# Performance work log

Measured on AMD Instinct MI355X. Metric: run time of the kernel, lower is better.

Reference implementation:

```python
import jax, jax.numpy as jnp
import numpy as np

N_NODES = 32768
NUM_EDGES = 524288
NUM_GRAPHS = 32
C = 128            # hidden channels
N_LAYERS = 3       # len(hidden_channels)-1
D_IN = 144         # 4 (op embedding dim) + 140
C_MID = 80         # mem1 out
C_OUT = 64         # mem2 out / classes
H1, K1N = 5, 10    # mem1 heads / clusters
H2, K2N = 5, 1     # mem2 heads / clusters
EPS = 1e-15


def _gatv2(x, src, dst, Wl, bl, Wr, br, att, cb):
    """GATv2Conv (heads=1, negative_slope=0.2), edges src->dst incl. self loops."""
    n = x.shape[0]
    xl = x @ Wl + bl                                  # source transform [N,C]
    xr = x @ Wr + br                                  # target transform [N,C]
    e = (jax.nn.leaky_relu(xl[src] + xr[dst], 0.2) @ att)  # [E]
    m = jax.ops.segment_max(e, dst, num_segments=n)   # segment softmax over in-edges
    ee = jnp.exp(e - m[dst])
    denom = jax.ops.segment_sum(ee, dst, num_segments=n)
    alpha = ee / denom[dst]
    out = jax.ops.segment_sum(alpha[:, None] * xl[src], dst, num_segments=n)
    return out + cb


def _bn(h, gamma, beta):
    # BatchNorm1d with batch statistics (training-mode forward), eps=1e-5
    mu = h.mean(0)
    var = h.var(0)
    return (h - mu) * jax.lax.rsqrt(var + 1e-5) * gamma + beta


def _mem_pool(xd, Kmem, W):
    # xd [B,N,C], Kmem [H,K,C]; Student-t kernel, tau=1 -> (1+d)^-1
    d = (jnp.sum(xd * xd, -1)[:, :, None, None]
         + jnp.sum(Kmem * Kmem, -1)[None, None]
         - 2.0 * jnp.einsum('bnc,hkc->bnhk', xd, Kmem))  # [B,N,H,K] sq. distances
    S = 1.0 / (1.0 + d)
    S = S / S.sum(-1, keepdims=True)   # normalize over clusters
    S = S.mean(2)                      # average heads -> [B,N,K]
    out = jnp.einsum('bnk,bnc->bkc', S, xd) @ W
    return out, S


def _kl_loss(S):
    S2 = S * S / S.sum(1, keepdims=True)
    den = S2.sum(2, keepdims=True)
    den = jnp.where(S.sum(2, keepdims=True) == 0.0, 1.0, den)
    P = jnp.maximum(S2 / den, EPS)
    Sc = jnp.maximum(S, EPS)
    # KLDivLoss(reduction='batchmean'), input = log(S)
    return jnp.sum(P * (jnp.log(P) - jnp.log(Sc))) / S.shape[0]


def setup_inputs():
    key = jax.random.key(0)
    ks = jax.random.split(key, 24)
    x = jax.random.normal(ks[0], (N_NODES, D_IN), jnp.float32)
    edge_index = jax.random.randint(ks[1], (2, NUM_EDGES), 0, N_NODES, jnp.int32)
    batch = (jnp.arange(N_NODES, dtype=jnp.int32) // (N_NODES // NUM_GRAPHS))
    s = 1.0 / np.sqrt(C)
    inp = {
        'x': x, 'edge_index': edge_index, 'batch': batch,
        'W_in': jax.random.normal(ks[2], (D_IN, C), jnp.float32) / np.sqrt(D_IN),
        'b_in': jnp.zeros((C,), jnp.float32),
        'bn_gamma': jnp.ones((N_LAYERS, C), jnp.float32),
        'bn_beta': jnp.zeros((N_LAYERS, C), jnp.float32),
        'Wl': jax.random.normal(ks[3], (N_LAYERS, C, C), jnp.float32) * s,
        'bl': jnp.zeros((N_LAYERS, C), jnp.float32),
        'Wr': jax.random.normal(ks[4], (N_LAYERS, C, C), jnp.float32) * s,
        'br': jnp.zeros((N_LAYERS, C), jnp.float32),
        'att': jax.random.normal(ks[5], (N_LAYERS, C), jnp.float32) * s,
        'conv_bias': jnp.zeros((N_LAYERS, C), jnp.float32),
        'K1': jax.random.normal(ks[6], (H1, K1N, C), jnp.float32),
        'Wm1': jax.random.normal(ks[7], (C, C_MID), jnp.float32) * s,
        'K2': jax.random.normal(ks[8], (H2, K2N, C_MID), jnp.float32),
        'Wm2': jax.random.normal(ks[9], (C_MID, C_OUT), jnp.float32) / np.sqrt(C_MID),
    }
    return inp


def reference(x, edge_index, batch, W_in, b_in, bn_gamma, bn_beta,
              Wl, bl, Wr, br, att, conv_bias, K1, Wm1, K2, Wm2):
    h = x @ W_in + b_in                               # self.linear
    loops = jnp.arange(N_NODES, dtype=edge_index.dtype)
    src = jnp.concatenate([edge_index[0], loops])     # GATv2 add_self_loops=True
    dst = jnp.concatenate([edge_index[1], loops])
    for l in range(N_LAYERS):                         # DeepGCNLayer block='res+'
        t = _bn(h, bn_gamma[l], bn_beta[l])
        t = jax.nn.leaky_relu(t, 0.01)
        # dropout: identity (deterministic reference)
        t = _gatv2(t, src, dst, Wl[l], bl[l], Wr[l], br[l], att[l], conv_bias[l])
        h = h + t
    per = N_NODES // NUM_GRAPHS
    xd = h.reshape(NUM_GRAPHS, per, C)                # to_dense_batch (equal-size graphs)
    x1, S1 = _mem_pool(xd, K1, Wm1)                   # [B,10,80]
    x1 = jax.nn.leaky_relu(x1, 0.01)
    x2, S2 = _mem_pool(x1, K2, Wm2)                   # [B,1,64]
    logits = jax.nn.log_softmax(x2.squeeze(1), -1)    # [B,64]
    return logits, _kl_loss(S1) + _kl_loss(S2)
```

## Files before the change

kernel.cpp:

```cpp
#include <hip/hip_runtime.h>
#include <math.h>

#define N_NODES   32768
#define NUM_EDGES 524288
#define NUM_GRAPHS 32
#define PER_G     1024
#define C         128
#define D_IN      144
#define C_MID     80
#define C_OUT     64
#define NL        3

#define WS_H    0
#define WS_XL   16777216
#define WS_XR   25165824
#define WS_CSR  33554432
#define WS_DEG  35651584
#define WS_OFF  35782656
#define WS_CUR  35913728
#define WS_BNP  36044800
#define WS_SC   38141952
#define WS_SH   38142464
#define WS_S1   38142976
#define WS_CS   39453696
#define WS_PP   39454976
#define WS_X1   44697856
#define WS_KL   44800256

using short8 = __attribute__((ext_vector_type(8))) short;
using f32x4  = __attribute__((ext_vector_type(4))) float;

__device__ __forceinline__ float wave_sum(float v) {
  #pragma unroll
  for (int m = 1; m < 64; m <<= 1) v += __shfl_xor(v, m, 64);
  return v;
}

__device__ __forceinline__ float lrelu2(float v) { return fmaxf(v, 0.2f * v); }

__device__ __forceinline__ unsigned short f2bf(float f) {
  union { float f; unsigned u; } c; c.f = f;
  unsigned r = (c.u + 0x7FFFu + ((c.u >> 16) & 1u)) >> 16;
  return (unsigned short)r;
}
__device__ __forceinline__ float bflo(unsigned u) {
  union { unsigned u; float f; } c; c.u = u << 16; return c.f;
}
__device__ __forceinline__ float bfhi(unsigned u) {
  union { unsigned u; float f; } c; c.u = u & 0xFFFF0000u; return c.f;
}

__global__ void k_count(const int* __restrict__ dst, int* __restrict__ deg) {
  int e = blockIdx.x * 256 + threadIdx.x;
  if (e < NUM_EDGES) atomicAdd(&deg[dst[e]], 1);
}

__global__ __launch_bounds__(1024) void k_scan(const int* __restrict__ deg, int* __restrict__ off) {
  __shared__ int part[1024];
  int t = threadIdx.x;
  int base = t * 32;
  int s = 0;
  #pragma unroll
  for (int i = 0; i < 32; i++) s += deg[base + i];
  part[t] = s;
  __syncthreads();
  for (int d = 1; d < 1024; d <<= 1) {
    int v = (t >= d) ? part[t - d] : 0;
    __syncthreads();
    part[t] += v;
    __syncthreads();
  }
  int run = (t == 0) ? 0 : part[t - 1];
  for (int i = 0; i < 32; i++) { off[base + i] = run; run += deg[base + i]; }
}

__global__ void k_fill(const int* __restrict__ src, const int* __restrict__ dst,
                       const int* __restrict__ off, int* __restrict__ cur,
                       int* __restrict__ csr) {
  int e = blockIdx.x * 256 + threadIdx.x;
  if (e < NUM_EDGES) {
    int d = dst[e];
    int p = atomicAdd(&cur[d], 1);
    csr[off[d] + p] = src[e];
  }
}

__global__ __launch_bounds__(256) void k_lin_mfma(const float* __restrict__ x,
    const float* __restrict__ W, const float* __restrict__ bias, float* __restrict__ h) {
  __shared__ __align__(16) char smem[61440];
  char* tA = smem;
  char* tB = smem + 20480;
  int n0 = blockIdx.x * 64;
  int tid = threadIdx.x;
  for (int t = 0; t < 32; t++) {
    int cp = tid & 127;
    int node = t * 2 + (tid >> 7);
    if (cp < 80) {
      unsigned pkv = 0;
      if (cp < 72) {
        float2 xv = *(const float2*)&x[(size_t)(n0 + node) * D_IN + 2 * cp];
        pkv = ((unsigned)f2bf(xv.y) << 16) | f2bf(xv.x);
      }
      int byte = node * 320 + ((4 * cp) ^ ((node & 3) << 4));
      *(unsigned*)(tA + byte) = pkv;
    }
  }
  {
    int col = tid & 127, hh = tid >> 7;
    for (int t = 0; t < 40; t++) {
      int kp = t * 2 + hh;
      float w0 = (2 * kp < D_IN) ? W[(size_t)(2 * kp) * C + col] : 0.f;
      float w1 = (2 * kp + 1 < D_IN) ? W[(size_t)(2 * kp + 1) * C + col] : 0.f;
      unsigned pkv = ((unsigned)f2bf(w1) << 16) | f2bf(w0);
      int byte = col * 320 + ((4 * kp) ^ ((col & 3) << 4));
      *(unsigned*)(tB + byte) = pkv;
    }
  }
  __syncthreads();
  int l = tid & 63, w = tid >> 6;
  f32x4 acc[8];
  #pragma unroll
  for (int f = 0; f < 8; f++) acc[f] = (f32x4){0.f, 0.f, 0.f, 0.f};
  int arow = w * 16 + (l & 15);
  #pragma unroll
  for (int ks = 0; ks < 5; ks++) {
    int kb = ks * 64 + (l >> 4) * 16;
    short8 a = *(const short8*)(tA + arow * 320 + (kb ^ ((arow & 3) << 4)));
    #pragma unroll
    for (int f = 0; f < 8; f++) {
      int col = f * 16 + (l & 15);
      short8 b = *(const short8*)(tB + col * 320 + (kb ^ ((col & 3) << 4)));
      acc[f] = __builtin_amdgcn_mfma_f32_16x16x32_bf16(a, b, acc[f], 0, 0, 0);
    }
  }
  int rowb = n0 + w * 16 + (l >> 4) * 4;
  #pragma unroll
  for (int f = 0; f < 8; f++) {
    int col = f * 16 + (l & 15);
    float bv = bias[col];
    #pragma unroll
    for (int r = 0; r < 4; r++)
      h[(size_t)(rowb + r) * C + col] = acc[f][r] + bv;
  }
}

__global__ __launch_bounds__(128) void k_bn_part(const float* __restrict__ h, float* __restrict__ part) {
  int b = blockIdx.x; int c = threadIdx.x;
  float s = 0.f, s2 = 0.f;
  int r0 = b * 128;
  for (int r = 0; r < 128; r++) {
    float v = h[(size_t)(r0 + r) * C + c];
    s += v; s2 += v * v;
  }
  part[b * C + c] = s;
  part[256 * C + b * C + c] = s2;
}

__global__ __launch_bounds__(1024) void k_bn_fin(const float* __restrict__ part,
    const float* __restrict__ gamma, const float* __restrict__ beta,
    float* __restrict__ sc, float* __restrict__ sh) {
  __shared__ float ls[8 * 128];
  __shared__ float ls2[8 * 128];
  int c = threadIdx.x & 127, g = threadIdx.x >> 7;
  float s = 0.f, s2 = 0.f;
  for (int i = 0; i < 32; i++) {
    int b = g * 32 + i;
    s += part[b * C + c];
    s2 += part[256 * C + b * C + c];
  }
  ls[g * 128 + c] = s;
  ls2[g * 128 + c] = s2;
  __syncthreads();
  if (g == 0) {
    double S = 0.0, S2 = 0.0;
    #pragma unroll
    for (int k = 0; k < 8; k++) { S += ls[k * 128 + c]; S2 += ls2[k * 128 + c]; }
    double m = S / (double)N_NODES;
    double var = S2 / (double)N_NODES - m * m;
    float rsig = (float)(1.0 / sqrt(var + 1e-5));
    float scv = rsig * gamma[c];
    sc[c] = scv;
    sh[c] = beta[c] - (float)m * scv;
  }
}

__device__ __forceinline__ void gemm_half(const char* tA, const char* tB,
    const float* bias, unsigned short* out, int n0, int tid) {
  int l = tid & 63, w = tid >> 6;
  f32x4 acc[8];
  #pragma unroll
  for (int f = 0; f < 8; f++) acc[f] = (f32x4){0.f, 0.f, 0.f, 0.f};
  int arow = w * 16 + (l & 15);
  #pragma unroll
  for (int ks = 0; ks < 4; ks++) {
    int kb = ks * 64 + (l >> 4) * 16;
    short8 a = *(const short8*)(tA + arow * 256 + (kb ^ ((arow & 7) << 4)));
    #pragma unroll
    for (int f = 0; f < 8; f++) {
      int col = f * 16 + (l & 15);
      short8 b = *(const short8*)(tB + col * 256 + (kb ^ ((col & 7) << 4)));
      acc[f] = __builtin_amdgcn_mfma_f32_16x16x32_bf16(a, b, acc[f], 0, 0, 0);
    }
  }
  int rowb = n0 + w * 16 + (l >> 4) * 4;
  #pragma unroll
  for (int f = 0; f < 8; f++) {
    int col = f * 16 + (l & 15);
    float bv = bias[col];
    #pragma unroll
    for (int r = 0; r < 4; r++)
      out[(size_t)(rowb + r) * C + col] = f2bf(acc[f][r] + bv);
  }
}

__device__ __forceinline__ void stage_B(char* tB, const float* __restrict__ W, int tid) {
  int col = tid & 127, hh = tid >> 7;
  for (int t = 0; t < 32; t++) {
    int kp = t * 2 + hh;
    float w0 = W[(size_t)(2 * kp) * C + col];
    float w1 = W[(size_t)(2 * kp + 1) * C + col];
    unsigned pkv = ((unsigned)f2bf(w1) << 16) | f2bf(w0);
    int byte = col * 256 + ((4 * kp) ^ ((col & 7) << 4));
    *(unsigned*)(tB + byte) = pkv;
  }
}

__global__ __launch_bounds__(256) void k_gemm_mfma(const float* __restrict__ h,
    const float* __restrict__ sc, const float* __restrict__ sh,
    const float* __restrict__ Wl, const float* __restrict__ bl,
    const float* __restrict__ Wr, const float* __restrict__ br,
    unsigned short* __restrict__ xl, unsigned short* __restrict__ xr) {
  __shared__ __align__(16) char smem[49152];
  char* tA = smem;
  char* tB = smem + 16384;
  int n0 = blockIdx.x * 64;
  int tid = threadIdx.x;
  for (int t = 0; t < 16; t++) {
    int item = t * 256 + tid;
    int node = item >> 6;
    int cp = item & 63;
    float2 hv = *(const float2*)&h[(size_t)(n0 + node) * C + 2 * cp];
    float2 scv = *(const float2*)&sc[2 * cp];
    float2 shv = *(const float2*)&sh[2 * cp];
    float t0 = hv.x * scv.x + shv.x; t0 = fmaxf(t0, 0.01f * t0);
    float t1 = hv.y * scv.y + shv.y; t1 = fmaxf(t1, 0.01f * t1);
    unsigned pkv = ((unsigned)f2bf(t1) << 16) | f2bf(t0);
    int byte = node * 256 + ((4 * cp) ^ ((node & 7) << 4));
    *(unsigned*)(tA + byte) = pkv;
  }
  stage_B(tB, Wl, tid);
  __syncthreads();
  gemm_half(tA, tB, bl, xl, n0, tid);
  __syncthreads();
  stage_B(tB, Wr, tid);
  __syncthreads();
  gemm_half(tA, tB, br, xr, n0, tid);
}

__global__ __launch_bounds__(256) void k_gat(float* __restrict__ h,
    const unsigned* __restrict__ xlb, const unsigned* __restrict__ xrb,
    const float* __restrict__ att, const float* __restrict__ cb,
    const int* __restrict__ off, const int* __restrict__ deg,
    const int* __restrict__ csr) {
  int tid = threadIdx.x;
  int lane = tid & 63;
  int w = tid >> 6;
  int half = lane >> 5;
  int q = lane & 31;
  int node = blockIdx.x * 8 + w * 2 + half;
  float4 a = *(const float4*)&att[q * 4];
  uint2 ur = *(const uint2*)&xrb[(size_t)node * 64 + q * 2];
  float xr0 = bflo(ur.x), xr1 = bfhi(ur.x), xr2 = bflo(ur.y), xr3 = bfhi(ur.y);
  uint2 us = *(const uint2*)&xlb[(size_t)node * 64 + q * 2];
  float acc0 = bflo(us.x), acc1 = bfhi(us.x), acc2 = bflo(us.y), acc3 = bfhi(us.y);
  float p0 = lrelu2(acc0 + xr0) * a.x + lrelu2(acc1 + xr1) * a.y
           + lrelu2(acc2 + xr2) * a.z + lrelu2(acc3 + xr3) * a.w;
  #pragma unroll
  for (int mm = 1; mm < 32; mm <<= 1) p0 += __shfl_xor(p0, mm, 64);
  float m = p0;
  float ssum = 1.f;
  int o = off[node], dg = deg[node];
  int dgmax = max(dg, __shfl_xor(dg, 32, 64));
  for (int j = 0; j < dgmax; j += 4) {
    int i0 = o + ((j + 0 < dg) ? j + 0 : 0);
    int i1 = o + ((j + 1 < dg) ? j + 1 : 0);
    int i2 = o + ((j + 2 < dg) ? j + 2 : 0);
    int i3 = o + ((j + 3 < dg) ? j + 3 : 0);
    int s0 = csr[i0], s1 = csr[i1], s2 = csr[i2], s3 = csr[i3];
    uint2 u0 = *(const uint2*)&xlb[(size_t)s0 * 64 + q * 2];
    uint2 u1 = *(const uint2*)&xlb[(size_t)s1 * 64 + q * 2];
    uint2 u2 = *(const uint2*)&xlb[(size_t)s2 * 64 + q * 2];
    uint2 u3 = *(const uint2*)&xlb[(size_t)s3 * 64 + q * 2];
    float y00 = bflo(u0.x), y01 = bfhi(u0.x), y02 = bflo(u0.y), y03 = bfhi(u0.y);
    float y10 = bflo(u1.x), y11 = bfhi(u1.x), y12 = bflo(u1.y), y13 = bfhi(u1.y);
    float y20 = bflo(u2.x), y21 = bfhi(u2.x), y22 = bflo(u2.y), y23 = bfhi(u2.y);
    float y30 = bflo(u3.x), y31 = bfhi(u3.x), y32 = bflo(u3.y), y33 = bfhi(u3.y);
    float t0 = lrelu2(y00 + xr0) * a.x + lrelu2(y01 + xr1) * a.y
             + lrelu2(y02 + xr2) * a.z + lrelu2(y03 + xr3) * a.w;
    float t1 = lrelu2(y10 + xr0) * a.x + lrelu2(y11 + xr1) * a.y
             + lrelu2(y12 + xr2) * a.z + lrelu2(y13 + xr3) * a.w;
    float t2 = lrelu2(y20 + xr0) * a.x + lrelu2(y21 + xr1) * a.y
             + lrelu2(y22 + xr2) * a.z + lrelu2(y23 + xr3) * a.w;
    float t3 = lrelu2(y30 + xr0) * a.x + lrelu2(y31 + xr1) * a.y
             + lrelu2(y32 + xr2) * a.z + lrelu2(y33 + xr3) * a.w;
    #pragma unroll
    for (int mm = 1; mm < 32; mm <<= 1) {
      t0 += __shfl_xor(t0, mm, 64);
      t1 += __shfl_xor(t1, mm, 64);
      t2 += __shfl_xor(t2, mm, 64);
      t3 += __shfl_xor(t3, mm, 64);
    }
    t0 = (j + 0 < dg) ? t0 : -1e30f;
    t1 = (j + 1 < dg) ? t1 : -1e30f;
    t2 = (j + 2 < dg) ? t2 : -1e30f;
    t3 = (j + 3 < dg) ? t3 : -1e30f;
    {
      float nm = fmaxf(m, t0); float f = __expf(m - nm); float p = __expf(t0 - nm);
      ssum = fmaf(ssum, f, p);
      acc0 = fmaf(acc0, f, p * y00); acc1 = fmaf(acc1, f, p * y01);
      acc2 = fmaf(acc2, f, p * y02); acc3 = fmaf(acc3, f, p * y03);
      m = nm;
    }
    {
      float nm = fmaxf(m, t1); float f = __expf(m - nm); float p = __expf(t1 - nm);
      ssum = fmaf(ssum, f, p);
      acc0 = fmaf(acc0, f, p * y10); acc1 = fmaf(acc1, f, p * y11);
      acc2 = fmaf(acc2, f, p * y12); acc3 = fmaf(acc3, f, p * y13);
      m = nm;
    }
    {
      float nm = fmaxf(m, t2); float f = __expf(m - nm); float p = __expf(t2 - nm);
      ssum = fmaf(ssum, f, p);
      acc0 = fmaf(acc0, f, p * y20); acc1 = fmaf(acc1, f, p * y21);
      acc2 = fmaf(acc2, f, p * y22); acc3 = fmaf(acc3, f, p * y23);
      m = nm;
    }
    {
      float nm = fmaxf(m, t3); float f = __expf(m - nm); float p = __expf(t3 - nm);
      ssum = fmaf(ssum, f, p);
      acc0 = fmaf(acc0, f, p * y30); acc1 = fmaf(acc1, f, p * y31);
      acc2 = fmaf(acc2, f, p * y32); acc3 = fmaf(acc3, f, p * y33);
      m = nm;
    }
  }
  float inv = 1.f / ssum;
  float4 cbv = *(const float4*)&cb[q * 4];
  float4 hv = *(float4*)&h[(size_t)node * C + q * 4];
  hv.x += acc0 * inv + cbv.x;
  hv.y += acc1 * inv + cbv.y;
  hv.z += acc2 * inv + cbv.z;
  hv.w += acc3 * inv + cbv.w;
  *(float4*)&h[(size_t)node * C + q * 4] = hv;
}

__global__ __launch_bounds__(320) void k_mem1(const float* __restrict__ h,
    const float* __restrict__ K1, float* __restrict__ S1, float* __restrict__ colsum) {
  __shared__ float dd[64 * 51];
  __shared__ float kn[50];
  int tid = threadIdx.x;
  int lane = tid & 63;
  int w = tid >> 6;
  int n0 = blockIdx.x * 64;
  if (tid < 50) {
    const float4* kr = reinterpret_cast<const float4*>(K1 + tid * C);
    float s = 0.f;
    for (int q = 0; q < 32; q++) {
      float4 kv = kr[q];
      s += kv.x * kv.x + kv.y * kv.y + kv.z * kv.z + kv.w * kv.w;
    }
    kn[tid] = s;
  }
  int wu = __builtin_amdgcn_readfirstlane(w);
  const float4* x4 = reinterpret_cast<const float4*>(h + (size_t)(n0 + lane) * C);
  const float4* K4 = reinterpret_cast<const float4*>(K1);
  float acc[10];
  #pragma unroll
  for (int it = 0; it < 10; it++) acc[it] = 0.f;
  float xn = 0.f;
  for (int q = 0; q < 32; q += 2) {
    float4 xa = x4[q], xb = x4[q + 1];
    xn += xa.x * xa.x + xa.y * xa.y + xa.z * xa.z + xa.w * xa.w
        + xb.x * xb.x + xb.y * xb.y + xb.z * xb.z + xb.w * xb.w;
    #pragma unroll
    for (int it = 0; it < 10; it++) {
      int j = wu + 5 * it;
      float4 ka = K4[j * 32 + q], kb = K4[j * 32 + q + 1];
      acc[it] += xa.x * ka.x + xa.y * ka.y + xa.z * ka.z + xa.w * ka.w
               + xb.x * kb.x + xb.y * kb.y + xb.z * kb.z + xb.w * kb.w;
    }
  }
  #pragma unroll
  for (int it = 0; it < 10; it++) dd[lane * 51 + wu + 5 * it] = acc[it];
  __syncthreads();
  if (tid < 64) {
    float sn[10];
    #pragma unroll
    for (int k = 0; k < 10; k++) sn[k] = 0.f;
    #pragma unroll
    for (int hd = 0; hd < 5; hd++) {
      float sh_[10]; float hs = 0.f;
      #pragma unroll
      for (int k = 0; k < 10; k++) {
        int j = hd * 10 + k;
        float dist = xn + kn[j] - 2.f * dd[tid * 51 + j];
        float s = 1.f / (1.f + dist);
        sh_[k] = s; hs += s;
      }
      float inv = 1.f / hs;
      #pragma unroll
      for (int k = 0; k < 10; k++) sn[k] += sh_[k] * inv;
    }
    int b = n0 >> 10;
    #pragma unroll
    for (int k = 0; k < 10; k++) {
      float v = 0.2f * sn[k];
      S1[(n0 + tid) * 10 + k] = v;
      float vs = wave_sum(v);
      if (tid == 0) atomicAdd(&colsum[b * 10 + k], vs);
    }
  }
}

__global__ __launch_bounds__(128) void k_pool1a(const float* __restrict__ h,
    const float* __restrict__ S1, float* __restrict__ pp) {
  int b = blockIdx.x >> 5, ch = blockIdx.x & 31;
  int c = threadIdx.x;
  float acc[10];
  #pragma unroll
  for (int k = 0; k < 10; k++) acc[k] = 0.f;
  int n0 = ch * 32;
  for (int n = 0; n < 32; n++) {
    int i = b * PER_G + n0 + n;
    float xv = h[(size_t)i * C + c];
    #pragma unroll
    for (int k = 0; k < 10; k++) acc[k] += S1[i * 10 + k] * xv;
  }
  #pragma unroll
  for (int k = 0; k < 10; k++) pp[(size_t)((b * 32 + ch) * 10 + k) * C + c] = acc[k];
}

__global__ __launch_bounds__(128) void k_pool1b(const float* __restrict__ pp,
    const float* __restrict__ Wm1, float* __restrict__ x1) {
  int bk = blockIdx.x; int b = bk / 10; int k = bk - b * 10;
  int c = threadIdx.x;
  __shared__ float red[C];
  float r = 0.f;
  for (int ch = 0; ch < 32; ch++) r += pp[(size_t)((b * 32 + ch) * 10 + k) * C + c];
  red[c] = r;
  __syncthreads();
  if (c < C_MID) {
    float o = 0.f;
    for (int mIdx = 0; mIdx < C; mIdx++) o += red[mIdx] * Wm1[mIdx * C_MID + c];
    o = fmaxf(o, 0.01f * o);
    x1[bk * C_MID + c] = o;
  }
}

__global__ __launch_bounds__(256) void k_kl1(const float* __restrict__ S1,
    const float* __restrict__ colsum, float* __restrict__ kl) {
  int i = blockIdx.x * 256 + threadIdx.x;
  int b = i >> 10;
  float s[10], q[10];
  float den = 0.f;
  #pragma unroll
  for (int k = 0; k < 10; k++) {
    s[k] = S1[i * 10 + k];
    q[k] = s[k] * s[k] / colsum[b * 10 + k];
    den += q[k];
  }
  float inv = 1.f / den;
  float term = 0.f;
  #pragma unroll
  for (int k = 0; k < 10; k++) {
    float P = fmaxf(q[k] * inv, 1e-15f);
    float Sc = fmaxf(s[k], 1e-15f);
    term += P * (logf(P) - logf(Sc));
  }
  term *= (1.f / (float)NUM_GRAPHS);
  term = wave_sum(term);
  if ((threadIdx.x & 63) == 0) atomicAdd(kl, term);
}

__global__ __launch_bounds__(128) void k_mem2(const float* __restrict__ x1,
    const float* __restrict__ Wm2, const float* __restrict__ kl, float* __restrict__ out) {
  int b = blockIdx.x;
  __shared__ float t80[C_MID];
  int tid = threadIdx.x;
  if (tid < C_MID) {
    float s = 0.f;
    #pragma unroll
    for (int k = 0; k < 10; k++) s += x1[(b * 10 + k) * C_MID + tid];
    t80[tid] = s;
  }
  __syncthreads();
  if (tid < C_OUT) {
    float o = 0.f;
    for (int mIdx = 0; mIdx < C_MID; mIdx++) o += t80[mIdx] * Wm2[mIdx * C_OUT + tid];
    float mx = o;
    #pragma unroll
    for (int d = 1; d < 64; d <<= 1) mx = fmaxf(mx, __shfl_xor(mx, d, 64));
    float p = expf(o - mx);
    float sum = p;
    #pragma unroll
    for (int d = 1; d < 64; d <<= 1) sum += __shfl_xor(sum, d, 64);
    out[b * C_OUT + tid] = o - mx - logf(sum);
  }
  if (b == 0 && tid == 127) out[NUM_GRAPHS * C_OUT] = kl[0];
}

extern "C" void kernel_launch(void* const* d_in, const int* in_sizes, int n_in,
                              void* d_out, int out_size, void* d_ws, size_t ws_size,
                              hipStream_t stream) {
  const float* x    = (const float*)d_in[0];
  const int*   ei   = (const int*)d_in[1];
  const float* W_in = (const float*)d_in[3];
  const float* b_in = (const float*)d_in[4];
  const float* bn_g = (const float*)d_in[5];
  const float* bn_b = (const float*)d_in[6];
  const float* Wl   = (const float*)d_in[7];
  const float* bl   = (const float*)d_in[8];
  const float* Wr   = (const float*)d_in[9];
  const float* br   = (const float*)d_in[10];
  const float* att  = (const float*)d_in[11];
  const float* cb   = (const float*)d_in[12];
  const float* K1   = (const float*)d_in[13];
  const float* Wm1  = (const float*)d_in[14];
  const float* Wm2  = (const float*)d_in[16];
  float* out = (float*)d_out;

  char* ws = (char*)d_ws;
  float* h    = (float*)(ws + WS_H);
  unsigned short* xlp = (unsigned short*)(ws + WS_XL);
  unsigned short* xrp = (unsigned short*)(ws + WS_XR);
  int*   csr  = (int*)(ws + WS_CSR);
  int*   deg  = (int*)(ws + WS_DEG);
  int*   off  = (int*)(ws + WS_OFF);
  int*   cur  = (int*)(ws + WS_CUR);
  float* bnp  = (float*)(ws + WS_BNP);
  float* scv  = (float*)(ws + WS_SC);
  float* shv  = (float*)(ws + WS_SH);
  float* S1p  = (float*)(ws + WS_S1);
  float* cs   = (float*)(ws + WS_CS);
  float* pp   = (float*)(ws + WS_PP);
  float* x1p  = (float*)(ws + WS_X1);
  float* klp  = (float*)(ws + WS_KL);

  const int* srcp = ei;
  const int* dstp = ei + NUM_EDGES;

  hipMemsetAsync(deg, 0, N_NODES * sizeof(int), stream);
  hipMemsetAsync(cur, 0, N_NODES * sizeof(int), stream);
  hipMemsetAsync(cs, 0, NUM_GRAPHS * 10 * sizeof(float), stream);
  hipMemsetAsync(klp, 0, sizeof(float), stream);

  k_count<<<NUM_EDGES / 256, 256, 0, stream>>>(dstp, deg);
  k_scan<<<1, 1024, 0, stream>>>(deg, off);
  k_fill<<<NUM_EDGES / 256, 256, 0, stream>>>(srcp, dstp, off, cur, csr);

  k_lin_mfma<<<N_NODES / 64, 256, 0, stream>>>(x, W_in, b_in, h);

  for (int l = 0; l < NL; l++) {
    k_bn_part<<<256, 128, 0, stream>>>(h, bnp);
    k_bn_fin<<<1, 1024, 0, stream>>>(bnp, bn_g + l * C, bn_b + l * C, scv, shv);
    k_gemm_mfma<<<N_NODES / 64, 256, 0, stream>>>(h, scv, shv,
        Wl + l * C * C, bl + l * C,
        Wr + l * C * C, br + l * C,
        xlp, xrp);
    k_gat<<<N_NODES / 8, 256, 0, stream>>>(h, (const unsigned*)xlp, (const unsigned*)xrp,
        att + l * C, cb + l * C, off, deg, csr);
  }

  k_mem1<<<N_NODES / 64, 320, 0, stream>>>(h, K1, S1p, cs);
  k_pool1a<<<NUM_GRAPHS * 32, 128, 0, stream>>>(h, S1p, pp);
  k_pool1b<<<NUM_GRAPHS * 10, 128, 0, stream>>>(pp, Wm1, x1p);
  k_kl1<<<N_NODES / 256, 256, 0, stream>>>(S1p, cs, klp);
  k_mem2<<<NUM_GRAPHS, 128, 0, stream>>>(x1p, Wm2, klp, out);
}
```

Measured before the change: 314.2 us.

## Fuse BatchNorm statistics into producer kernels and widen GAT edge batching

Removes the separate k_bn_part pass by accumulating per-channel sum and sum-of-squares inside k_lin_mfma and k_gat. Each block reduces through LDS atomics, then adds into 32 global bins with atomics, and k_bn_fin reads the bins and clears them for the next layer. The GAT loop also gathers 8 neighbours per iteration instead of 4 to expose more memory-level parallelism. The four memsets are merged into one over a regrouped workspace layout. The cost is extra LDS and global atomics plus float-atomic ordering nondeterminism in the statistics.

```diff
diff --git a/kernel.cpp b/kernel.cpp
--- a/kernel.cpp
+++ b/kernel.cpp
@@ -10,22 +10,25 @@
 #define C_MID     80
 #define C_OUT     64
 #define NL        3
+#define NBINS     32
 
 #define WS_H    0
 #define WS_XL   16777216
 #define WS_XR   25165824
 #define WS_CSR  33554432
 #define WS_DEG  35651584
-#define WS_OFF  35782656
-#define WS_CUR  35913728
-#define WS_BNP  36044800
-#define WS_SC   38141952
-#define WS_SH   38142464
-#define WS_S1   38142976
-#define WS_CS   39453696
-#define WS_PP   39454976
-#define WS_X1   44697856
-#define WS_KL   44800256
+#define WS_CUR  35782656
+#define WS_PART 35913728
+#define WS_CS   35946496
+#define WS_KL   35947776
+#define WS_ZERO_BASE WS_DEG
+#define WS_ZERO_SIZE (35947780 - 35651584)
+#define WS_SC   35948544
+#define WS_SH   35949056
+#define WS_S1   35949568
+#define WS_PP   37260288
+#define WS_X1   42503168
+#define WS_OFF  42605568
 
 using short8 = __attribute__((ext_vector_type(8))) short;
 using f32x4  = __attribute__((ext_vector_type(4))) float;
@@ -86,12 +89,16 @@
 }
 
 __global__ __launch_bounds__(256) void k_lin_mfma(const float* __restrict__ x,
-    const float* __restrict__ W, const float* __restrict__ bias, float* __restrict__ h) {
+    const float* __restrict__ W, const float* __restrict__ bias,
+    float* __restrict__ h, float* __restrict__ part) {
   __shared__ __align__(16) char smem[61440];
+  __shared__ float lsum[128];
+  __shared__ float lsum2[128];
   char* tA = smem;
   char* tB = smem + 20480;
   int n0 = blockIdx.x * 64;
   int tid = threadIdx.x;
+  if (tid < 128) { lsum[tid] = 0.f; lsum2[tid] = 0.f; }
   for (int t = 0; t < 32; t++) {
     int cp = tid & 127;
     int node = t * 2 + (tid >> 7);
@@ -138,50 +145,43 @@
   for (int f = 0; f < 8; f++) {
     int col = f * 16 + (l & 15);
     float bv = bias[col];
-    #pragma unroll
-    for (int r = 0; r < 4; r++)
-      h[(size_t)(rowb + r) * C + col] = acc[f][r] + bv;
-  }
-}
-
-__global__ __launch_bounds__(128) void k_bn_part(const float* __restrict__ h, float* __restrict__ part) {
-  int b = blockIdx.x; int c = threadIdx.x;
-  float s = 0.f, s2 = 0.f;
-  int r0 = b * 128;
-  for (int r = 0; r < 128; r++) {
-    float v = h[(size_t)(r0 + r) * C + c];
-    s += v; s2 += v * v;
-  }
-  part[b * C + c] = s;
-  part[256 * C + b * C + c] = s2;
-}
-
-__global__ __launch_bounds__(1024) void k_bn_fin(const float* __restrict__ part,
+    float s = 0.f, s2 = 0.f;
+    #pragma unroll
+    for (int r = 0; r < 4; r++) {
+      float v = acc[f][r] + bv;
+      h[(size_t)(rowb + r) * C + col] = v;
+      s += v; s2 += v * v;
+    }
+    atomicAdd(&lsum[col], s);
+    atomicAdd(&lsum2[col], s2);
+  }
+  __syncthreads();
+  if (tid < 128) {
+    int bin = blockIdx.x & (NBINS - 1);
+    atomicAdd(&part[bin * 256 + tid], lsum[tid]);
+    atomicAdd(&part[bin * 256 + 128 + tid], lsum2[tid]);
+  }
+}
+
+__global__ __launch_bounds__(256) void k_bn_fin(float* __restrict__ part,
     const float* __restrict__ gamma, const float* __restrict__ beta,
     float* __restrict__ sc, float* __restrict__ sh) {
-  __shared__ float ls[8 * 128];
-  __shared__ float ls2[8 * 128];
-  int c = threadIdx.x & 127, g = threadIdx.x >> 7;
-  float s = 0.f, s2 = 0.f;
-  for (int i = 0; i < 32; i++) {
-    int b = g * 32 + i;
-    s += part[b * C + c];
-    s2 += part[256 * C + b * C + c];
-  }
-  ls[g * 128 + c] = s;
-  ls2[g * 128 + c] = s2;
-  __syncthreads();
-  if (g == 0) {
+  int tid = threadIdx.x;
+  if (tid < 128) {
     double S = 0.0, S2 = 0.0;
-    #pragma unroll
-    for (int k = 0; k < 8; k++) { S += ls[k * 128 + c]; S2 += ls2[k * 128 + c]; }
+    for (int b = 0; b < NBINS; b++) {
+      S += (double)part[b * 256 + tid];
+      S2 += (double)part[b * 256 + 128 + tid];
+    }
     double m = S / (double)N_NODES;
     double var = S2 / (double)N_NODES - m * m;
     float rsig = (float)(1.0 / sqrt(var + 1e-5));
-    float scv = rsig * gamma[c];
-    sc[c] = scv;
-    sh[c] = beta[c] - (float)m * scv;
-  }
+    float scv = rsig * gamma[tid];
+    sc[tid] = scv;
+    sh[tid] = beta[tid] - (float)m * scv;
+  }
+  __syncthreads();
+  for (int i = tid; i < NBINS * 256; i += 256) part[i] = 0.f;
 }
 
 __device__ __forceinline__ void gemm_half(const char* tA, const char* tB,
@@ -261,8 +261,14 @@
     const unsigned* __restrict__ xlb, const unsigned* __restrict__ xrb,
     const float* __restrict__ att, const float* __restrict__ cb,
     const int* __restrict__ off, const int* __restrict__ deg,
-    const int* __restrict__ csr) {
+    const int* __restrict__ csr, float* __restrict__ part) {
+  __shared__ float gsum[128];
+  __shared__ float gsum2[128];
   int tid = threadIdx.x;
+  if (part) {
+    if (tid < 128) { gsum[tid] = 0.f; gsum2[tid] = 0.f; }
+    __syncthreads();
+  }
   int lane = tid & 63;
   int w = tid >> 6;
   int half = lane >> 5;
@@ -281,65 +287,41 @@
   float ssum = 1.f;
   int o = off[node], dg = deg[node];
   int dgmax = max(dg, __shfl_xor(dg, 32, 64));
-  for (int j = 0; j < dgmax; j += 4) {
-    int i0 = o + ((j + 0 < dg) ? j + 0 : 0);
-    int i1 = o + ((j + 1 < dg) ? j + 1 : 0);
-    int i2 = o + ((j + 2 < dg) ? j + 2 : 0);
-    int i3 = o + ((j + 3 < dg) ? j + 3 : 0);
-    int s0 = csr[i0], s1 = csr[i1], s2 = csr[i2], s3 = csr[i3];
-    uint2 u0 = *(const uint2*)&xlb[(size_t)s0 * 64 + q * 2];
-    uint2 u1 = *(const uint2*)&xlb[(size_t)s1 * 64 + q * 2];
-    uint2 u2 = *(const uint2*)&xlb[(size_t)s2 * 64 + q * 2];
-    uint2 u3 = *(const uint2*)&xlb[(size_t)s3 * 64 + q * 2];
-    float y00 = bflo(u0.x), y01 = bfhi(u0.x), y02 = bflo(u0.y), y03 = bfhi(u0.y);
-    float y10 = bflo(u1.x), y11 = bfhi(u1.x), y12 = bflo(u1.y), y13 = bfhi(u1.y);
-    float y20 = bflo(u2.x), y21 = bfhi(u2.x), y22 = bflo(u2.y), y23 = bfhi(u2.y);
-    float y30 = bflo(u3.x), y31 = bfhi(u3.x), y32 = bflo(u3.y), y33 = bfhi(u3.y);
-    float t0 = lrelu2(y00 + xr0) * a.x + lrelu2(y01 + xr1) * a.y
-             + lrelu2(y02 + xr2) * a.z + lrelu2(y03 + xr3) * a.w;
-    float t1 = lrelu2(y10 + xr0) * a.x + lrelu2(y11 + xr1) * a.y
-             + lrelu2(y12 + xr2) * a.z + lrelu2(y13 + xr3) * a.w;
-    float t2 = lrelu2(y20 + xr0) * a.x + lrelu2(y21 + xr1) * a.y
-             + lrelu2(y22 + xr2) * a.z + lrelu2(y23 + xr3) * a.w;
-    float t3 = lrelu2(y30 + xr0) * a.x + lrelu2(y31 + xr1) * a.y
-             + lrelu2(y32 + xr2) * a.z + lrelu2(y33 + xr3) * a.w;
+  for (int j = 0; j < dgmax; j += 8) {
+    int sidx[8];
+    uint2 u[8];
+    #pragma unroll
+    for (int e = 0; e < 8; e++) {
+      int jj = j + e;
+      sidx[e] = csr[o + ((jj < dg) ? jj : 0)];
+    }
+    #pragma unroll
+    for (int e = 0; e < 8; e++)
+      u[e] = *(const uint2*)&xlb[(size_t)sidx[e] * 64 + q * 2];
+    float y0[8], y1[8], y2[8], y3[8], t[8];
+    #pragma unroll
+    for (int e = 0; e < 8; e++) {
+      y0[e] = bflo(u[e].x); y1[e] = bfhi(u[e].x);
+      y2[e] = bflo(u[e].y); y3[e] = bfhi(u[e].y);
+      t[e] = lrelu2(y0[e] + xr0) * a.x + lrelu2(y1[e] + xr1) * a.y
+           + lrelu2(y2[e] + xr2) * a.z + lrelu2(y3[e] + xr3) * a.w;
+    }
     #pragma unroll
     for (int mm = 1; mm < 32; mm <<= 1) {
-      t0 += __shfl_xor(t0, mm, 64);
-      t1 += __shfl_xor(t1, mm, 64);
-      t2 += __shfl_xor(t2, mm, 64);
-      t3 += __shfl_xor(t3, mm, 64);
-    }
-    t0 = (j + 0 < dg) ? t0 : -1e30f;
-    t1 = (j + 1 < dg) ? t1 : -1e30f;
-    t2 = (j + 2 < dg) ? t2 : -1e30f;
-    t3 = (j + 3 < dg) ? t3 : -1e30f;
-    {
-      float nm = fmaxf(m, t0); float f = __expf(m - nm); float p = __expf(t0 - nm);
+      #pragma unroll
+      for (int e = 0; e < 8; e++) t[e] += __shfl_xor(t[e], mm, 64);
+    }
+    #pragma unroll
+    for (int e = 0; e < 8; e++) {
+      float te = (j + e < dg) ? t[e] : -1e30f;
+      float nm = fmaxf(m, te);
+      float f = __expf(m - nm);
+      float p = __expf(te - nm);
       ssum = fmaf(ssum, f, p);
-      acc0 = fmaf(acc0, f, p * y00); acc1 = fmaf(acc1, f, p * y01);
-      acc2 = fmaf(acc2, f, p * y02); acc3 = fmaf(acc3, f, p * y03);
-      m = nm;
-    }
-    {
-      float nm = fmaxf(m, t1); float f = __expf(m - nm); float p = __expf(t1 - nm);
-      ssum = fmaf(ssum, f, p);
-      acc0 = fmaf(acc0, f, p * y10); acc1 = fmaf(acc1, f, p * y11);
-      acc2 = fmaf(acc2, f, p * y12); acc3 = fmaf(acc3, f, p * y13);
-      m = nm;
-    }
-    {
-      float nm = fmaxf(m, t2); float f = __expf(m - nm); float p = __expf(t2 - nm);
-      ssum = fmaf(ssum, f, p);
-      acc0 = fmaf(acc0, f, p * y20); acc1 = fmaf(acc1, f, p * y21);
-      acc2 = fmaf(acc2, f, p * y22); acc3 = fmaf(acc3, f, p * y23);
-      m = nm;
-    }
-    {
-      float nm = fmaxf(m, t3); float f = __expf(m - nm); float p = __expf(t3 - nm);
-      ssum = fmaf(ssum, f, p);
-      acc0 = fmaf(acc0, f, p * y30); acc1 = fmaf(acc1, f, p * y31);
-      acc2 = fmaf(acc2, f, p * y32); acc3 = fmaf(acc3, f, p * y33);
+      acc0 = fmaf(acc0, f, p * y0[e]);
+      acc1 = fmaf(acc1, f, p * y1[e]);
+      acc2 = fmaf(acc2, f, p * y2[e]);
+      acc3 = fmaf(acc3, f, p * y3[e]);
       m = nm;
     }
   }
@@ -351,6 +333,22 @@
   hv.z += acc2 * inv + cbv.z;
   hv.w += acc3 * inv + cbv.w;
   *(float4*)&h[(size_t)node * C + q * 4] = hv;
+  if (part) {
+    atomicAdd(&gsum[q * 4 + 0], hv.x);
+    atomicAdd(&gsum[q * 4 + 1], hv.y);
+    atomicAdd(&gsum[q * 4 + 2], hv.z);
+    atomicAdd(&gsum[q * 4 + 3], hv.w);
+    atomicAdd(&gsum2[q * 4 + 0], hv.x * hv.x);
+    atomicAdd(&gsum2[q * 4 + 1], hv.y * hv.y);
+    atomicAdd(&gsum2[q * 4 + 2], hv.z * hv.z);
+    atomicAdd(&gsum2[q * 4 + 3], hv.w * hv.w);
+    __syncthreads();
+    if (tid < 128) {
+      int bin = blockIdx.x & (NBINS - 1);
+      atomicAdd(&part[bin * 256 + tid], gsum[tid]);
+      atomicAdd(&part[bin * 256 + 128 + tid], gsum2[tid]);
+    }
+  }
 }
 
 __global__ __launch_bounds__(320) void k_mem1(const float* __restrict__ h,
@@ -536,7 +534,7 @@
   int*   deg  = (int*)(ws + WS_DEG);
   int*   off  = (int*)(ws + WS_OFF);
   int*   cur  = (int*)(ws + WS_CUR);
-  float* bnp  = (float*)(ws + WS_BNP);
+  float* part = (float*)(ws + WS_PART);
   float* scv  = (float*)(ws + WS_SC);
   float* shv  = (float*)(ws + WS_SH);
   float* S1p  = (float*)(ws + WS_S1);
@@ -548,26 +546,23 @@
   const int* srcp = ei;
   const int* dstp = ei + NUM_EDGES;
 
-  hipMemsetAsync(deg, 0, N_NODES * sizeof(int), stream);
-  hipMemsetAsync(cur, 0, N_NODES * sizeof(int), stream);
-  hipMemsetAsync(cs, 0, NUM_GRAPHS * 10 * sizeof(float), stream);
-  hipMemsetAsync(klp, 0, sizeof(float), stream);
+  hipMemsetAsync(ws + WS_ZERO_BASE, 0, WS_ZERO_SIZE, stream);
 
   k_count<<<NUM_EDGES / 256, 256, 0, stream>>>(dstp, deg);
   k_scan<<<1, 1024, 0, stream>>>(deg, off);
   k_fill<<<NUM_EDGES / 256, 256, 0, stream>>>(srcp, dstp, off, cur, csr);
 
-  k_lin_mfma<<<N_NODES / 64, 256, 0, stream>>>(x, W_in, b_in, h);
+  k_lin_mfma<<<N_NODES / 64, 256, 0, stream>>>(x, W_in, b_in, h, part);
 
   for (int l = 0; l < NL; l++) {
-    k_bn_part<<<256, 128, 0, stream>>>(h, bnp);
-    k_bn_fin<<<1, 1024, 0, stream>>>(bnp, bn_g + l * C, bn_b + l * C, scv, shv);
+    k_bn_fin<<<1, 256, 0, stream>>>(part, bn_g + l * C, bn_b + l * C, scv, shv);
     k_gemm_mfma<<<N_NODES / 64, 256, 0, stream>>>(h, scv, shv,
         Wl + l * C * C, bl + l * C,
         Wr + l * C * C, br + l * C,
         xlp, xrp);
     k_gat<<<N_NODES / 8, 256, 0, stream>>>(h, (const unsigned*)xlp, (const unsigned*)xrp,
-        att + l * C, cb + l * C, off, deg, csr);
+        att + l * C, cb + l * C, off, deg, csr,
+        (l < NL - 1) ? part : (float*)nullptr);
   }
 
   k_mem1<<<N_NODES / 64, 320, 0, stream>>>(h, K1, S1p, cs);
```

Measured after the change: 385.7 us. +22.8%, slower.

## Fuse first BN statistics into input linear and bin BN partials atomically

Applied to the files above, without the earlier changes.

The input linear kernel now accumulates per-column sum and sum-of-squares while writing h, so the first layer skips its separate BN statistics pass. The BN partial kernel uses more, smaller blocks that atomically add into 32 bins, and the finalize kernel reads those bins and then zeroes them for the next layer. It also merges the four memsets into one, reorders the workspace to allow that, and vectorises the scan's loads and stores. The cost is extra LDS and global float atomics, plus summation order that is no longer deterministic.

```diff
diff --git a/kernel.cpp b/kernel.cpp
--- a/kernel.cpp
+++ b/kernel.cpp
@@ -10,22 +10,25 @@
 #define C_MID     80
 #define C_OUT     64
 #define NL        3
+#define NBINS     32
 
 #define WS_H    0
 #define WS_XL   16777216
 #define WS_XR   25165824
 #define WS_CSR  33554432
 #define WS_DEG  35651584
-#define WS_OFF  35782656
-#define WS_CUR  35913728
-#define WS_BNP  36044800
-#define WS_SC   38141952
-#define WS_SH   38142464
-#define WS_S1   38142976
-#define WS_CS   39453696
-#define WS_PP   39454976
-#define WS_X1   44697856
-#define WS_KL   44800256
+#define WS_CUR  35782656
+#define WS_PART 35913728
+#define WS_CS   35946496
+#define WS_KL   35947776
+#define WS_ZERO_BASE WS_DEG
+#define WS_ZERO_SIZE (35947780 - 35651584)
+#define WS_SC   35948544
+#define WS_SH   35949056
+#define WS_S1   35949568
+#define WS_PP   37260288
+#define WS_X1   42503168
+#define WS_OFF  42605568
 
 using short8 = __attribute__((ext_vector_type(8))) short;
 using f32x4  = __attribute__((ext_vector_type(4))) float;
@@ -59,19 +62,32 @@
   __shared__ int part[1024];
   int t = threadIdx.x;
   int base = t * 32;
+  int4 d[8];
+  const int4* dp = (const int4*)(deg + base);
+  #pragma unroll
+  for (int i = 0; i < 8; i++) d[i] = dp[i];
   int s = 0;
   #pragma unroll
-  for (int i = 0; i < 32; i++) s += deg[base + i];
+  for (int i = 0; i < 8; i++) s += d[i].x + d[i].y + d[i].z + d[i].w;
   part[t] = s;
   __syncthreads();
-  for (int d = 1; d < 1024; d <<= 1) {
-    int v = (t >= d) ? part[t - d] : 0;
+  for (int dd = 1; dd < 1024; dd <<= 1) {
+    int v = (t >= dd) ? part[t - dd] : 0;
     __syncthreads();
     part[t] += v;
     __syncthreads();
   }
   int run = (t == 0) ? 0 : part[t - 1];
-  for (int i = 0; i < 32; i++) { off[base + i] = run; run += deg[base + i]; }
+  int4* op = (int4*)(off + base);
+  #pragma unroll
+  for (int i = 0; i < 8; i++) {
+    int4 o;
+    o.x = run; run += d[i].x;
+    o.y = run; run += d[i].y;
+    o.z = run; run += d[i].z;
+    o.w = run; run += d[i].w;
+    op[i] = o;
+  }
 }
 
 __global__ void k_fill(const int* __restrict__ src, const int* __restrict__ dst,
@@ -86,12 +102,16 @@
 }
 
 __global__ __launch_bounds__(256) void k_lin_mfma(const float* __restrict__ x,
-    const float* __restrict__ W, const float* __restrict__ bias, float* __restrict__ h) {
+    const float* __restrict__ W, const float* __restrict__ bias,
+    float* __restrict__ h, float* __restrict__ part) {
   __shared__ __align__(16) char smem[61440];
+  __shared__ float lsum[128];
+  __shared__ float lsum2[128];
   char* tA = smem;
   char* tB = smem + 20480;
   int n0 = blockIdx.x * 64;
   int tid = threadIdx.x;
+  if (tid < 128) { lsum[tid] = 0.f; lsum2[tid] = 0.f; }
   for (int t = 0; t < 32; t++) {
     int cp = tid & 127;
     int node = t * 2 + (tid >> 7);
@@ -138,50 +158,56 @@
   for (int f = 0; f < 8; f++) {
     int col = f * 16 + (l & 15);
     float bv = bias[col];
-    #pragma unroll
-    for (int r = 0; r < 4; r++)
-      h[(size_t)(rowb + r) * C + col] = acc[f][r] + bv;
+    float s = 0.f, s2 = 0.f;
+    #pragma unroll
+    for (int r = 0; r < 4; r++) {
+      float v = acc[f][r] + bv;
+      h[(size_t)(rowb + r) * C + col] = v;
+      s += v; s2 += v * v;
+    }
+    atomicAdd(&lsum[col], s);
+    atomicAdd(&lsum2[col], s2);
+  }
+  __syncthreads();
+  if (tid < 128) {
+    int bin = blockIdx.x & (NBINS - 1);
+    atomicAdd(&part[bin * 256 + tid], lsum[tid]);
+    atomicAdd(&part[bin * 256 + 128 + tid], lsum2[tid]);
   }
 }
 
 __global__ __launch_bounds__(128) void k_bn_part(const float* __restrict__ h, float* __restrict__ part) {
   int b = blockIdx.x; int c = threadIdx.x;
   float s = 0.f, s2 = 0.f;
-  int r0 = b * 128;
-  for (int r = 0; r < 128; r++) {
+  int r0 = b * 64;
+  for (int r = 0; r < 64; r++) {
     float v = h[(size_t)(r0 + r) * C + c];
     s += v; s2 += v * v;
   }
-  part[b * C + c] = s;
-  part[256 * C + b * C + c] = s2;
-}
-
-__global__ __launch_bounds__(1024) void k_bn_fin(const float* __restrict__ part,
+  int bin = b & (NBINS - 1);
+  atomicAdd(&part[bin * 256 + c], s);
+  atomicAdd(&part[bin * 256 + 128 + c], s2);
+}
+
+__global__ __launch_bounds__(256) void k_bn_fin(float* __restrict__ part,
     const float* __restrict__ gamma, const float* __restrict__ beta,
     float* __restrict__ sc, float* __restrict__ sh) {
-  __shared__ float ls[8 * 128];
-  __shared__ float ls2[8 * 128];
-  int c = threadIdx.x & 127, g = threadIdx.x >> 7;
-  float s = 0.f, s2 = 0.f;
-  for (int i = 0; i < 32; i++) {
-    int b = g * 32 + i;
-    s += part[b * C + c];
-    s2 += part[256 * C + b * C + c];
-  }
-  ls[g * 128 + c] = s;
-  ls2[g * 128 + c] = s2;
-  __syncthreads();
-  if (g == 0) {
+  int tid = threadIdx.x;
+  if (tid < 128) {
     double S = 0.0, S2 = 0.0;
-    #pragma unroll
-    for (int k = 0; k < 8; k++) { S += ls[k * 128 + c]; S2 += ls2[k * 128 + c]; }
+    for (int b = 0; b < NBINS; b++) {
+      S += (double)part[b * 256 + tid];
+      S2 += (double)part[b * 256 + 128 + tid];
+    }
     double m = S / (double)N_NODES;
     double var = S2 / (double)N_NODES - m * m;
     float rsig = (float)(1.0 / sqrt(var + 1e-5));
-    float scv = rsig * gamma[c];
-    sc[c] = scv;
-    sh[c] = beta[c] - (float)m * scv;
-  }
+    float scv = rsig * gamma[tid];
+    sc[tid] = scv;
+    sh[tid] = beta[tid] - (float)m * scv;
+  }
+  __syncthreads();
+  for (int i = tid; i < NBINS * 256; i += 256) part[i] = 0.f;
 }
 
 __device__ __forceinline__ void gemm_half(const char* tA, const char* tB,
@@ -536,7 +562,7 @@
   int*   deg  = (int*)(ws + WS_DEG);
   int*   off  = (int*)(ws + WS_OFF);
   int*   cur  = (int*)(ws + WS_CUR);
-  float* bnp  = (float*)(ws + WS_BNP);
+  float* part = (float*)(ws + WS_PART);
   float* scv  = (float*)(ws + WS_SC);
   float* shv  = (float*)(ws + WS_SH);
   float* S1p  = (float*)(ws + WS_S1);
@@ -548,20 +574,17 @@
   const int* srcp = ei;
   const int* dstp = ei + NUM_EDGES;
 
-  hipMemsetAsync(deg, 0, N_NODES * sizeof(int), stream);
-  hipMemsetAsync(cur, 0, N_NODES * sizeof(int), stream);
-  hipMemsetAsync(cs, 0, NUM_GRAPHS * 10 * sizeof(float), stream);
-  hipMemsetAsync(klp, 0, sizeof(float), stream);
+  hipMemsetAsync(ws + WS_ZERO_BASE, 0, WS_ZERO_SIZE, stream);
 
   k_count<<<NUM_EDGES / 256, 256, 0, stream>>>(dstp, deg);
   k_scan<<<1, 1024, 0, stream>>>(deg, off);
   k_fill<<<NUM_EDGES / 256, 256, 0, stream>>>(srcp, dstp, off, cur, csr);
 
-  k_lin_mfma<<<N_NODES / 64, 256, 0, stream>>>(x, W_in, b_in, h);
+  k_lin_mfma<<<N_NODES / 64, 256, 0, stream>>>(x, W_in, b_in, h, part);
 
   for (int l = 0; l < NL; l++) {
-    k_bn_part<<<256, 128, 0, stream>>>(h, bnp);
-    k_bn_fin<<<1, 1024, 0, stream>>>(bnp, bn_g + l * C, bn_b + l * C, scv, shv);
+    if (l > 0) k_bn_part<<<N_NODES / 64, 128, 0, stream>>>(h, part);
+    k_bn_fin<<<1, 256, 0, stream>>>(part, bn_g + l * C, bn_b + l * C, scv, shv);
     k_gemm_mfma<<<N_NODES / 64, 256, 0, stream>>>(h, scv, shv,
         Wl + l * C * C, bl + l * C,
         Wr + l * C * C, br + l * C,
```

Result: no change. 314.2 us (+0.0%).
